# Kernel tuning notes

Measured on AMD Instinct MI355X. Metric: run time of the kernel, lower is better.

## Reference

```python
import jax, jax.numpy as jnp
import numpy as np

B, C, H, W = 8, 96, 224, 224
WS, SS, NH = 7, 3, 3          # window size, shift size, num heads
HD = C // NH                  # head dim = 32
N = WS * WS                   # tokens per window = 49
MLP_H = 4 * C
EPS = 1e-5


def _rel_pos_index():
    coords = np.stack(np.meshgrid(np.arange(WS), np.arange(WS), indexing='ij'))  # (2, ws, ws)
    cf = coords.reshape(2, -1)                       # (2, N)
    rel = cf[:, :, None] - cf[:, None, :]            # (2, N, N)
    rel = rel.transpose(1, 2, 0).copy()              # (N, N, 2)
    rel[:, :, 0] += WS - 1
    rel[:, :, 1] += WS - 1
    rel[:, :, 0] *= 2 * WS - 1
    return rel.sum(-1)                               # (N, N) int


def _attn_mask():
    # Swin shifted-window mask: (num_windows, N, N) with 0 / -100
    img = np.zeros((H, W), np.float32)
    cnt = 0
    for hs in (slice(0, -WS), slice(-WS, -SS), slice(-SS, None)):
        for ws_ in (slice(0, -WS), slice(-WS, -SS), slice(-SS, None)):
            img[hs, ws_] = cnt
            cnt += 1
    mw = img.reshape(H // WS, WS, W // WS, WS).transpose(0, 2, 1, 3).reshape(-1, N)
    m = mw[:, None, :] - mw[:, :, None]
    return np.where(m != 0, np.float32(-100.0), np.float32(0.0))


def setup_inputs() -> dict:
    key = jax.random.key(0)
    ks = jax.random.split(key, 8)
    s = 0.02
    return {
        "x": jax.random.normal(ks[0], (B, C, H, W), jnp.float32),
        "attn_mask": jnp.asarray(_attn_mask()),
        "norm1_g": jnp.ones((C,), jnp.float32),
        "norm1_b": jnp.zeros((C,), jnp.float32),
        "qkv_w": jax.random.normal(ks[1], (C, 3 * C), jnp.float32) * s,
        "qkv_b": jnp.zeros((3 * C,), jnp.float32),
        "rpb": jax.random.normal(ks[2], ((2 * WS - 1) ** 2, NH), jnp.float32) * s,
        "proj_w": jax.random.normal(ks[3], (C, C), jnp.float32) * s,
        "proj_b": jnp.zeros((C,), jnp.float32),
        "norm2_g": jnp.ones((C,), jnp.float32),
        "norm2_b": jnp.zeros((C,), jnp.float32),
        "fc1_w": jax.random.normal(ks[4], (C, MLP_H), jnp.float32) * s,
        "fc1_b": jnp.zeros((MLP_H,), jnp.float32),
        "fc2_w": jax.random.normal(ks[5], (MLP_H, C), jnp.float32) * s,
        "fc2_b": jnp.zeros((C,), jnp.float32),
    }


def _ln(x, g, b):
    mu = jnp.mean(x, axis=-1, keepdims=True)
    var = jnp.var(x, axis=-1, keepdims=True)
    return (x - mu) * jax.lax.rsqrt(var + EPS) * g + b


def reference(x, attn_mask, norm1_g, norm1_b, qkv_w, qkv_b, rpb, proj_w, proj_b,
              norm2_g, norm2_b, fc1_w, fc1_b, fc2_w, fc2_b):
    shortcut = x
    # (B,C,H,W) -> (B,HW,C) -> LN -> (B,H,W,C)
    xl = jnp.transpose(x, (0, 2, 3, 1)).reshape(B, H * W, C)
    xl = _ln(xl, norm1_g, norm1_b).reshape(B, H, W, C)
    # H,W divisible by WS: pad_r = pad_b = 0
    sx = jnp.roll(xl, (-SS, -SS), axis=(1, 2))
    # window partition -> (B*nW, N, C)
    xw = sx.reshape(B, H // WS, WS, W // WS, WS, C).transpose(0, 1, 3, 2, 4, 5).reshape(-1, N, C)
    B_ = xw.shape[0]
    nW = B_ // B
    qkv = (xw @ qkv_w + qkv_b).reshape(B_, N, 3, NH, HD).transpose(2, 0, 3, 1, 4)
    q = qkv[0] * (HD ** -0.5)
    k, v = qkv[1], qkv[2]
    attn = jnp.einsum('bhnd,bhmd->bhnm', q, k)           # (B_, NH, N, N)
    rel_idx = jnp.asarray(_rel_pos_index())
    bias = rpb[rel_idx.reshape(-1)].reshape(N, N, NH).transpose(2, 0, 1)  # (NH, N, N)
    attn = attn + bias[None]
    attn = attn.reshape(B, nW, NH, N, N) + attn_mask[None, :, None]
    attn = jax.nn.softmax(attn.reshape(B_, NH, N, N), axis=-1)
    out = jnp.einsum('bhnm,bhmd->bhnd', attn, v).transpose(0, 2, 1, 3).reshape(B_, N, C)
    out = out @ proj_w + proj_b
    # window reverse -> (B, H, W, C)
    out = out.reshape(B, H // WS, W // WS, WS, WS, C).transpose(0, 1, 3, 2, 4, 5).reshape(B, H, W, C)
    out = jnp.roll(out, (SS, SS), axis=(1, 2))
    # faithful to original: permute(0,1,3,2) then raw reshape to (B,C,H,W)
    out = jnp.transpose(out, (0, 1, 3, 2)).reshape(B, C, H, W)
    x1 = shortcut + out
    # MLP branch, faithful: permute(0,1,3,2) then raw reshape to (B,HW,C)
    xm = jnp.transpose(x1, (0, 1, 3, 2)).reshape(B, H * W, C)
    xm = _ln(xm, norm2_g, norm2_b)
    xm = jax.nn.gelu(xm @ fc1_w + fc1_b, approximate=False) @ fc2_w + fc2_b
    xm = xm.reshape(B, C, H, W)
    return x1 + xm
```

## Files before the change

### kernel.cpp

```cpp
#include <hip/hip_runtime.h>
#include <hip/hip_bf16.h>


typedef __attribute__((ext_vector_type(4))) float f32x4;
typedef __attribute__((ext_vector_type(8))) short s16x8;

constexpr int B_ = 8;
constexpr int M_ = 96 * 224 * 224;

__device__ __forceinline__ ushort f2bs(float f) {
    __hip_bfloat16 h = __float2bfloat16(f);
    ushort u; __builtin_memcpy(&u, &h, 2); return u;
}
__device__ __forceinline__ float bs2f(ushort u) {
    __hip_bfloat16 h; __builtin_memcpy(&h, &u, 2); return __bfloat162float(h);
}
__device__ __forceinline__ f32x4 mfma16(s16x8 a, s16x8 b, f32x4 c) {
    return __builtin_amdgcn_mfma_f32_16x16x32_bf16(a, b, c, 0, 0, 0);
}
__device__ __forceinline__ float gelu_f(float v) {
    float s  = v * 0.70710678118654752f;
    float as = fabsf(s);
    float t  = __builtin_amdgcn_rcpf(fmaf(0.3275911f, as, 1.0f));
    float p  = fmaf(fmaf(fmaf(fmaf(1.061405429f, t, -1.453152027f), t,
                   1.421413741f), t, -0.284496736f), t, 0.254829592f) * t;
    float y  = 1.0f - p * __expf(-s * s);
    float er = copysignf(y, s);
    return 0.5f * v * (1.0f + er);
}

__global__ __launch_bounds__(256) void prep_kernel(
    const float* __restrict__ qkvw, const float* __restrict__ projw,
    const float* __restrict__ w1,   const float* __restrict__ w2,
    ushort* __restrict__ wq, ushort* __restrict__ wp,
    ushort* __restrict__ wf1, ushort* __restrict__ wf2)
{
    int i = blockIdx.x * 256 + threadIdx.x;
    if (i < 27648) { int n = i / 96, k = i % 96;  wq[i]  = f2bs(qkvw[k * 288 + n]); }
    if (i < 9216)  { int n = i / 96, k = i % 96;  wp[i]  = f2bs(projw[k * 96 + n]); }
    if (i < 36864) {
        int n = i / 96,  k = i % 96;   wf1[i] = f2bs(w1[k * 384 + n]);
        int n2 = i / 384, k2 = i % 384; wf2[i] = f2bs(w2[k2 * 96 + n2]);
    }
}

__global__ __launch_bounds__(256) void attn_kernel(
    const float* __restrict__ x,
    const float* __restrict__ amask,
    const float* __restrict__ n1g, const float* __restrict__ n1b,
    const float* __restrict__ qkvb,
    const float* __restrict__ rpb,
    const float* __restrict__ projb,
    const ushort* __restrict__ wq, const ushort* __restrict__ wp,
    ushort* __restrict__ x1)
{
    __shared__ __align__(16) ushort T[64][104];
    __shared__ __align__(16) ushort K[64][104];
    __shared__ __align__(16) ushort vT[96][72];
    __shared__ __align__(16) ushort Pws[4][16][72];
    __shared__ float rpbs[512];

    const int tid  = threadIdx.x;
    const int wave = tid >> 6, lane = tid & 63;
    const int cu   = lane & 15;
    const int g4   = lane >> 4;
    const int gk8  = g4 << 3;
    const int gr4  = g4 << 2;

    const int blk = (blockIdx.x & 7) * 1024 + (blockIdx.x >> 3);
    const int b   = blk >> 10;
    const int wi  = blk & 1023;
    const int wh  = wi >> 5, ww = wi & 31;
    const int bM  = b * M_;
    const bool need_mask = (wh == 31) || (ww == 31);

    for (int i = tid; i < 507; i += 256) rpbs[i] = rpb[i];

    const int t49 = tid % 49;
    const int g5  = tid / 49;
    int hh_s = 0, wc_s = 0;
    if (tid < 245) {
        int i = t49 / 7, j = t49 % 7;
        hh_s = wh * 7 + i + 3; if (hh_s >= 224) hh_s -= 224;
        wc_s = ww * 7 + j + 3; if (wc_s >= 224) wc_s -= 224;
    }

    if (tid < 245) {
        const float* xp = x + bM + g5 * 50176 + hh_s * 224 + wc_s;
        ushort* dT = &T[t49][g5];
        #pragma unroll 4
        for (int c = g5; c < 96; c += 5) {
            *dT = f2bs(*xp);
            xp += 5 * 50176; dT += 5;
        }
    }
    {
        uint* z = (uint*)&T[49][0];
        for (int i = tid; i < 780; i += 256) z[i] = 0u;
    }
    __syncthreads();

    if (tid < 196) {
        int t = tid >> 2, s = tid & 3;
        float sum = 0.f, sq = 0.f;
        float vv[24];
        #pragma unroll
        for (int i = 0; i < 24; ++i) {
            vv[i] = bs2f(T[t][s * 24 + i]);
            sum += vv[i]; sq += vv[i] * vv[i];
        }
        sum += __shfl_xor(sum, 1); sq += __shfl_xor(sq, 1);
        sum += __shfl_xor(sum, 2); sq += __shfl_xor(sq, 2);
        float mu   = sum * (1.0f / 96.0f);
        float rstd = rsqrtf(sq * (1.0f / 96.0f) - mu * mu + 1e-5f);
        #pragma unroll
        for (int i = 0; i < 24; ++i) {
            int c = s * 24 + i;
            T[t][c] = f2bs((vv[i] - mu) * rstd * n1g[c] + n1b[c]);
        }
    }
    __syncthreads();

    const int ar = (wave << 4) | cu;
    const int tr = (wave << 4) + gr4;

    {
        s16x8 a0 = *(const s16x8*)&T[ar][gk8];
        s16x8 a1 = *(const s16x8*)&T[ar][32 + gk8];
        s16x8 a2 = *(const s16x8*)&T[ar][64 + gk8];
        f32x4 qreg[6];

        auto qkv_store = [&](int nt, f32x4 acc) {
            int nc = (nt << 4) | cu;
            float bias = qkvb[nc];
            if (nt < 6) {
                #pragma unroll
                for (int r = 0; r < 4; ++r)
                    qreg[nt][r] = (acc[r] + bias) * 0.17677669529663689f;
            } else if (nt < 12) {
                #pragma unroll
                for (int r = 0; r < 4; ++r) K[tr + r][nc - 96] = f2bs(acc[r] + bias);
            } else {
                int d = nc - 192;
                ushort4 pk;
                pk.x = f2bs(acc[0] + bias); pk.y = f2bs(acc[1] + bias);
                pk.z = f2bs(acc[2] + bias); pk.w = f2bs(acc[3] + bias);
                *(ushort4*)&vT[d][tr] = pk;
            }
        };

        s16x8 e0, e1, e2, o0, o1, o2;
        {
            const ushort* bp = wq + cu * 96 + gk8;
            e0 = *(const s16x8*)(bp);
            e1 = *(const s16x8*)(bp + 32);
            e2 = *(const s16x8*)(bp + 64);
        }
        #pragma unroll
        for (int p = 0; p < 9; ++p) {
            const int ntE = 2 * p, ntO = 2 * p + 1;
            {
                int nc = (ntO << 4) | cu;
                const ushort* bp = wq + nc * 96 + gk8;
                o0 = *(const s16x8*)(bp);
                o1 = *(const s16x8*)(bp + 32);
                o2 = *(const s16x8*)(bp + 64);
            }
            {
                f32x4 acc = {0.f, 0.f, 0.f, 0.f};
                acc = mfma16(a0, e0, acc);
                acc = mfma16(a1, e1, acc);
                acc = mfma16(a2, e2, acc);
                qkv_store(ntE, acc);
            }
            if (p < 8) {
                int nc = ((ntE + 2) << 4) | cu;
                const ushort* bp = wq + nc * 96 + gk8;
                e0 = *(const s16x8*)(bp);
                e1 = *(const s16x8*)(bp + 32);
                e2 = *(const s16x8*)(bp + 64);
            }
            {
                f32x4 acc = {0.f, 0.f, 0.f, 0.f};
                acc = mfma16(a0, o0, acc);
                acc = mfma16(a1, o1, acc);
                acc = mfma16(a2, o2, acc);
                qkv_store(ntO, acc);
            }
        }
        #pragma unroll
        for (int qn = 0; qn < 6; ++qn)
            #pragma unroll
            for (int r = 0; r < 4; ++r)
                T[tr + r][(qn << 4) | cu] = f2bs(qreg[qn][r]);
    }
    __syncthreads();

    int u7d[4], u7m[4];
    #pragma unroll
    for (int ut = 0; ut < 4; ++ut) {
        int u = (ut << 4) | cu;
        u7d[ut] = u / 7; u7m[ut] = u % 7;
    }
    s16x8 ones8;
    #pragma unroll
    for (int i = 0; i < 8; ++i) ones8[i] = (short)0x3F80;

    #pragma unroll
    for (int it = 0; it < 3; ++it) {
        const int hh = it;
        const int t0r = tr;

        s16x8 aq = *(const s16x8*)&T[ar][(hh << 5) + gk8];
        s16x8 bk0 = *(const s16x8*)&K[(0 << 4) | cu][(hh << 5) + gk8];
        s16x8 bk1 = *(const s16x8*)&K[(1 << 4) | cu][(hh << 5) + gk8];
        s16x8 bk2 = *(const s16x8*)&K[(2 << 4) | cu][(hh << 5) + gk8];
        s16x8 bk3 = *(const s16x8*)&K[(3 << 4) | cu][(hh << 5) + gk8];
        f32x4 z = {0.f, 0.f, 0.f, 0.f};
        f32x4 sa[4];
        sa[0] = mfma16(aq, bk0, z);
        sa[1] = mfma16(aq, bk1, z);
        sa[2] = mfma16(aq, bk2, z);
        sa[3] = mfma16(aq, bk3, z);

        #pragma unroll
        for (int ut = 0; ut < 4; ++ut) {
            int u = (ut << 4) | cu;
            #pragma unroll
            for (int r = 0; r < 4; ++r) {
                int t = t0r + r;
                float s = sa[ut][r];
                if (t < 49 && u < 49) {
                    int dr = t / 7 - u7d[ut] + 6, dc = t % 7 - u7m[ut] + 6;
                    s += rpbs[(dr * 13 + dc) * 3 + hh];
                    if (need_mask) s += amask[(wi * 49 + t) * 49 + u];
                } else if (u >= 49) {
                    s = -1e30f;
                }
                sa[ut][r] = s;
            }
        }
        #pragma unroll
        for (int r = 0; r < 4; ++r) {
            float m = fmaxf(fmaxf(sa[0][r], sa[1][r]), fmaxf(sa[2][r], sa[3][r]));
            m = fmaxf(m, __shfl_xor(m, 1)); m = fmaxf(m, __shfl_xor(m, 2));
            m = fmaxf(m, __shfl_xor(m, 4)); m = fmaxf(m, __shfl_xor(m, 8));
            sa[0][r] = __expf(sa[0][r] - m);
            sa[1][r] = __expf(sa[1][r] - m);
            sa[2][r] = __expf(sa[2][r] - m);
            sa[3][r] = __expf(sa[3][r] - m);
        }
        #pragma unroll
        for (int ut = 0; ut < 4; ++ut) {
            int u = (ut << 4) | cu;
            #pragma unroll
            for (int r = 0; r < 4; ++r) Pws[wave][gr4 + r][u] = f2bs(sa[ut][r]);
        }
        s16x8 pa0 = *(const s16x8*)&Pws[wave][cu][gk8];
        s16x8 pa1 = *(const s16x8*)&Pws[wave][cu][32 + gk8];
        f32x4 accd = {0.f, 0.f, 0.f, 0.f};
        accd = mfma16(pa0, ones8, accd);
        accd = mfma16(pa1, ones8, accd);
        int d0 = (hh << 5) + cu, d1 = d0 + 16;
        s16x8 bv00 = *(const s16x8*)&vT[d0][gk8];
        s16x8 bv01 = *(const s16x8*)&vT[d0][32 + gk8];
        s16x8 bv10 = *(const s16x8*)&vT[d1][gk8];
        s16x8 bv11 = *(const s16x8*)&vT[d1][32 + gk8];
        f32x4 acco0 = {0.f, 0.f, 0.f, 0.f}, acco1 = {0.f, 0.f, 0.f, 0.f};
        acco0 = mfma16(pa0, bv00, acco0);
        acco0 = mfma16(pa1, bv01, acco0);
        acco1 = mfma16(pa0, bv10, acco1);
        acco1 = mfma16(pa1, bv11, acco1);
        float inv[4];
        #pragma unroll
        for (int r = 0; r < 4; ++r) inv[r] = __builtin_amdgcn_rcpf(accd[r]);
        #pragma unroll
        for (int r = 0; r < 4; ++r) {
            T[t0r + r][(hh << 5) + cu]      = f2bs(acco0[r] * inv[r]);
            T[t0r + r][(hh << 5) + 16 + cu] = f2bs(acco1[r] * inv[r]);
        }
    }

    {
        s16x8 a0 = *(const s16x8*)&T[ar][gk8];
        s16x8 a1 = *(const s16x8*)&T[ar][32 + gk8];
        s16x8 a2 = *(const s16x8*)&T[ar][64 + gk8];

        s16x8 e0, e1, e2, o0, o1, o2;
        {
            const ushort* bp = wp + cu * 96 + gk8;
            e0 = *(const s16x8*)(bp);
            e1 = *(const s16x8*)(bp + 32);
            e2 = *(const s16x8*)(bp + 64);
        }
        #pragma unroll
        for (int p = 0; p < 3; ++p) {
            const int ntE = 2 * p, ntO = 2 * p + 1;
            {
                int nc = (ntO << 4) | cu;
                const ushort* bp = wp + nc * 96 + gk8;
                o0 = *(const s16x8*)(bp);
                o1 = *(const s16x8*)(bp + 32);
                o2 = *(const s16x8*)(bp + 64);
            }
            {
                int nc = (ntE << 4) | cu;
                f32x4 acc = {0.f, 0.f, 0.f, 0.f};
                acc = mfma16(a0, e0, acc);
                acc = mfma16(a1, e1, acc);
                acc = mfma16(a2, e2, acc);
                float bias = projb[nc];
                #pragma unroll
                for (int r = 0; r < 4; ++r) T[tr + r][nc] = f2bs(acc[r] + bias);
            }
            if (p < 2) {
                int nc = ((ntE + 2) << 4) | cu;
                const ushort* bp = wp + nc * 96 + gk8;
                e0 = *(const s16x8*)(bp);
                e1 = *(const s16x8*)(bp + 32);
                e2 = *(const s16x8*)(bp + 64);
            }
            {
                int nc = (ntO << 4) | cu;
                f32x4 acc = {0.f, 0.f, 0.f, 0.f};
                acc = mfma16(a0, o0, acc);
                acc = mfma16(a1, o1, acc);
                acc = mfma16(a2, o2, acc);
                float bias = projb[nc];
                #pragma unroll
                for (int r = 0; r < 4; ++r) T[tr + r][nc] = f2bs(acc[r] + bias);
            }
        }
    }
    __syncthreads();

    if (tid < 245) {
        const int base = bM + (hh_s * 96 + g5) * 224 + wc_s;
        const float* xp = x + base;
        ushort* dx = x1 + base;
        const ushort* Tp = &T[t49][g5];
        #pragma unroll 4
        for (int c = g5; c < 96; c += 5) {
            *dx = f2bs(*xp + bs2f(*Tp));
            xp += 5 * 224; dx += 5 * 224; Tp += 5;
        }
    }
}

__global__ __launch_bounds__(256) void transpose_kernel(
    const ushort* __restrict__ x1, ushort* __restrict__ x1p)
{
    __shared__ ushort tile[32][36];
    const int id      = blockIdx.x;
    const int tile_id = id % 49;
    const int slab    = id / 49;
    const int h0 = (tile_id / 7) * 32;
    const int w0 = (tile_id % 7) * 32;
    const ushort* src = x1  + slab * 50176;
    ushort*       dst = x1p + slab * 50176;

    const int i = threadIdx.x >> 3;
    const int j = (threadIdx.x & 7) * 4;

    *(ushort4*)&tile[i][j] = *(const ushort4*)&src[(h0 + i) * 224 + w0 + j];
    __syncthreads();
    ushort4 v;
    v.x = tile[j][i]; v.y = tile[j + 1][i]; v.z = tile[j + 2][i]; v.w = tile[j + 3][i];
    *(ushort4*)&dst[(w0 + i) * 224 + h0 + j] = v;
}

template <bool CLEAN>
__device__ __forceinline__ void ln_token(
    const ushort* __restrict__ xsrc, int tok, int gk8,
    const float* __restrict__ n2g, const float* __restrict__ n2b,
    s16x8& a0, s16x8& a1, s16x8& a2)
{
    float vals[24];
    if (CLEAN) {
        const ushort* base = xsrc + tok * 96 + gk8;
        s16x8 r0 = *(const s16x8*)(base);
        s16x8 r1 = *(const s16x8*)(base + 32);
        s16x8 r2 = *(const s16x8*)(base + 64);
        #pragma unroll
        for (int i = 0; i < 8; ++i) {
            vals[i]      = bs2f((ushort)r0[i]);
            vals[8 + i]  = bs2f((ushort)r1[i]);
            vals[16 + i] = bs2f((ushort)r2[i]);
        }
    } else {
        int bb = tok / 50176;
        int tl = tok % 50176;
        #pragma unroll
        for (int s = 0; s < 3; ++s)
            #pragma unroll
            for (int i = 0; i < 8; ++i) {
                int p = tl * 96 + gk8 + s * 32 + i;
                int c = p / 50176, rem = p % 50176;
                int w = rem / 224, h = rem % 224;
                vals[s * 8 + i] = bs2f(xsrc[bb * M_ + c * 50176 + h * 224 + w]);
            }
    }
    float sum = 0.f, sq = 0.f;
    #pragma unroll
    for (int i = 0; i < 24; ++i) { sum += vals[i]; sq += vals[i] * vals[i]; }
    sum += __shfl_xor(sum, 16); sq += __shfl_xor(sq, 16);
    sum += __shfl_xor(sum, 32); sq += __shfl_xor(sq, 32);
    float mu   = sum * (1.0f / 96.0f);
    float rstd = rsqrtf(sq * (1.0f / 96.0f) - mu * mu + 1e-5f);
    #pragma unroll
    for (int i = 0; i < 8; ++i) {
        int c0 = gk8 + i, c1 = gk8 + 32 + i, c2 = gk8 + 64 + i;
        a0[i] = (short)f2bs((vals[i]      - mu) * rstd * n2g[c0] + n2b[c0]);
        a1[i] = (short)f2bs((vals[8 + i]  - mu) * rstd * n2g[c1] + n2b[c1]);
        a2[i] = (short)f2bs((vals[16 + i] - mu) * rstd * n2g[c2] + n2b[c2]);
    }
}

template <bool CLEAN>
__global__ __launch_bounds__(256) void mlp_kernel(
    const ushort* __restrict__ xsrc,
    const ushort* __restrict__ x1flat,
    const float* __restrict__ n2g, const float* __restrict__ n2b,
    const float* __restrict__ b1v, const float* __restrict__ b2v,
    const ushort* __restrict__ wf1, const ushort* __restrict__ wf2,
    float* __restrict__ out)
{
    __shared__ __align__(16) ushort hS[4][2][32][40];

    const int tid  = threadIdx.x;
    const int wave = tid >> 6, lane = tid & 63;
    const int cu   = lane & 15;
    const int g4   = lane >> 4;
    const int gk8  = g4 << 3;
    const int gr4  = g4 << 2;
    const int t0g  = blockIdx.x * 128;
    const int tokA = t0g + (wave << 5) + cu;
    const int tokB = tokA + 16;

    s16x8 aA0, aA1, aA2, aB0, aB1, aB2;
    ln_token<CLEAN>(xsrc, tokA, gk8, n2g, n2b, aA0, aA1, aA2);
    ln_token<CLEAN>(xsrc, tokB, gk8, n2g, n2b, aB0, aB1, aB2);

    auto fc1_step = [&](int s, int buf) {
        #pragma unroll
        for (int half = 0; half < 2; ++half) {
            int nc = ((2 * s + half) << 4) | cu;
            const ushort* bp = wf1 + nc * 96 + gk8;
            s16x8 b0 = *(const s16x8*)(bp);
            s16x8 b1 = *(const s16x8*)(bp + 32);
            s16x8 b2 = *(const s16x8*)(bp + 64);
            float bias = b1v[nc];
            f32x4 accA = {0.f, 0.f, 0.f, 0.f};
            accA = mfma16(aA0, b0, accA);
            accA = mfma16(aA1, b1, accA);
            accA = mfma16(aA2, b2, accA);
            f32x4 accB = {0.f, 0.f, 0.f, 0.f};
            accB = mfma16(aB0, b0, accB);
            accB = mfma16(aB1, b1, accB);
            accB = mfma16(aB2, b2, accB);
            #pragma unroll
            for (int r = 0; r < 4; ++r) {
                hS[wave][buf][gr4 + r][(half << 4) | cu]      = f2bs(gelu_f(accA[r] + bias));
                hS[wave][buf][16 + gr4 + r][(half << 4) | cu] = f2bs(gelu_f(accB[r] + bias));
            }
        }
    };

    f32x4 oaccA[6], oaccB[6];
    #pragma unroll
    for (int nt2 = 0; nt2 < 6; ++nt2) {
        oaccA[nt2] = (f32x4){0.f, 0.f, 0.f, 0.f};
        oaccB[nt2] = (f32x4){0.f, 0.f, 0.f, 0.f};
    }

    fc1_step(0, 0);
    for (int s = 0; s < 12; ++s) {
        int buf = s & 1;
        s16x8 haA = *(const s16x8*)&hS[wave][buf][cu][gk8];
        s16x8 haB = *(const s16x8*)&hS[wave][buf][16 + cu][gk8];
        if (s < 11) fc1_step(s + 1, buf ^ 1);
        #pragma unroll
        for (int nt2 = 0; nt2 < 6; ++nt2) {
            int nc2 = (nt2 << 4) | cu;
            s16x8 bv = *(const s16x8*)&wf2[nc2 * 384 + s * 32 + gk8];
            oaccA[nt2] = mfma16(haA, bv, oaccA[nt2]);
            oaccB[nt2] = mfma16(haB, bv, oaccB[nt2]);
        }
    }

    const int trow = (wave << 5) + gr4;
    #pragma unroll
    for (int nt2 = 0; nt2 < 6; ++nt2) {
        int nc2 = (nt2 << 4) | cu;
        float bias = b2v[nc2];
        #pragma unroll
        for (int r = 0; r < 4; ++r) {
            int GA = (t0g + trow + r) * 96 + nc2;
            out[GA] = bias + oaccA[nt2][r] + bs2f(x1flat[GA]);
            int GB = GA + 16 * 96;
            out[GB] = bias + oaccB[nt2][r] + bs2f(x1flat[GB]);
        }
    }
}

extern "C" void kernel_launch(void* const* d_in, const int* in_sizes, int n_in,
                              void* d_out, int out_size, void* d_ws, size_t ws_size,
                              hipStream_t stream) {
    const float* x      = (const float*)d_in[0];
    const float* amask  = (const float*)d_in[1];
    const float* n1g    = (const float*)d_in[2];
    const float* n1b    = (const float*)d_in[3];
    const float* qkvw   = (const float*)d_in[4];
    const float* qkvb   = (const float*)d_in[5];
    const float* rpb    = (const float*)d_in[6];
    const float* projw  = (const float*)d_in[7];
    const float* projb  = (const float*)d_in[8];
    const float* n2g    = (const float*)d_in[9];
    const float* n2b    = (const float*)d_in[10];
    const float* w1     = (const float*)d_in[11];
    const float* b1     = (const float*)d_in[12];
    const float* w2     = (const float*)d_in[13];
    const float* b2     = (const float*)d_in[14];

    char* ws = (char*)d_ws;
    ushort* wq  = (ushort*)(ws);
    ushort* wp  = (ushort*)(ws + 55296);
    ushort* wf1 = (ushort*)(ws + 73728);
    ushort* wf2 = (ushort*)(ws + 147456);
    ushort* x1  = (ushort*)(ws + 262144);
    ushort* x1p = (ushort*)(ws + 77332480);
    float* out = (float*)d_out;

    const bool clean = (ws_size >= (size_t)154402816);

    prep_kernel<<<dim3(144), dim3(256), 0, stream>>>(qkvw, projw, w1, w2, wq, wp, wf1, wf2);

    attn_kernel<<<dim3(8192), dim3(256), 0, stream>>>(
        x, amask, n1g, n1b, qkvb, rpb, projb, wq, wp, x1);

    if (clean) {
        transpose_kernel<<<dim3(37632), dim3(256), 0, stream>>>(x1, x1p);
        mlp_kernel<true><<<dim3(3136), dim3(256), 0, stream>>>(
            x1p, x1, n2g, n2b, b1, b2, wf1, wf2, out);
    } else {
        mlp_kernel<false><<<dim3(3136), dim3(256), 0, stream>>>(
            x1, x1, n2g, n2b, b1, b2, wf1, wf2, out);
    }
}
```

Before: 612.5 us.

## Process two adjacent windows per attention block with register prefetch of next window

New measurement: 627.6 us. 2.5% more time.

```diff
diff --git a/kernel.cpp b/kernel.cpp
--- a/kernel.cpp
+++ b/kernel.cpp
@@ -44,7 +44,7 @@
     }
 }
 
-__global__ __launch_bounds__(256) void attn_kernel(
+__global__ __launch_bounds__(256, 3) void attn_kernel(
     const float* __restrict__ x,
     const float* __restrict__ amask,
     const float* __restrict__ n1g, const float* __restrict__ n1b,
@@ -67,134 +67,28 @@
     const int gk8  = g4 << 3;
     const int gr4  = g4 << 2;
 
-    const int blk = (blockIdx.x & 7) * 1024 + (blockIdx.x >> 3);
-    const int b   = blk >> 10;
-    const int wi  = blk & 1023;
-    const int wh  = wi >> 5, ww = wi & 31;
-    const int bM  = b * M_;
-    const bool need_mask = (wh == 31) || (ww == 31);
+    const int pblk = (blockIdx.x & 7) * 512 + (blockIdx.x >> 3);
+    const int b    = pblk >> 9;
+    const int pr   = pblk & 511;
+    const int wh   = pr >> 4;
+    const int ww0  = (pr & 15) << 1;
+    const int bM   = b * M_;
 
     for (int i = tid; i < 507; i += 256) rpbs[i] = rpb[i];
 
     const int t49 = tid % 49;
     const int g5  = tid / 49;
-    int hh_s = 0, wc_s = 0;
-    if (tid < 245) {
-        int i = t49 / 7, j = t49 % 7;
-        hh_s = wh * 7 + i + 3; if (hh_s >= 224) hh_s -= 224;
-        wc_s = ww * 7 + j + 3; if (wc_s >= 224) wc_s -= 224;
-    }
-
-    if (tid < 245) {
-        const float* xp = x + bM + g5 * 50176 + hh_s * 224 + wc_s;
-        ushort* dT = &T[t49][g5];
-        #pragma unroll 4
-        for (int c = g5; c < 96; c += 5) {
-            *dT = f2bs(*xp);
-            xp += 5 * 50176; dT += 5;
-        }
-    }
-    {
-        uint* z = (uint*)&T[49][0];
-        for (int i = tid; i < 780; i += 256) z[i] = 0u;
-    }
-    __syncthreads();
-
-    if (tid < 196) {
-        int t = tid >> 2, s = tid & 3;
-        float sum = 0.f, sq = 0.f;
-        float vv[24];
-        #pragma unroll
-        for (int i = 0; i < 24; ++i) {
-            vv[i] = bs2f(T[t][s * 24 + i]);
-            sum += vv[i]; sq += vv[i] * vv[i];
-        }
-        sum += __shfl_xor(sum, 1); sq += __shfl_xor(sq, 1);
-        sum += __shfl_xor(sum, 2); sq += __shfl_xor(sq, 2);
-        float mu   = sum * (1.0f / 96.0f);
-        float rstd = rsqrtf(sq * (1.0f / 96.0f) - mu * mu + 1e-5f);
-        #pragma unroll
-        for (int i = 0; i < 24; ++i) {
-            int c = s * 24 + i;
-            T[t][c] = f2bs((vv[i] - mu) * rstd * n1g[c] + n1b[c]);
-        }
-    }
-    __syncthreads();
+    const bool vld = tid < 245;
+    int hh_s = 0, wc0 = 0, wc1 = 0;
+    if (vld) {
+        int i7 = t49 / 7, j7 = t49 % 7;
+        hh_s = wh * 7 + i7 + 3;  if (hh_s >= 224) hh_s -= 224;
+        wc0  = ww0 * 7 + j7 + 3; if (wc0 >= 224) wc0 -= 224;
+        wc1  = wc0 + 7;          if (wc1 >= 224) wc1 -= 224;
+    }
 
     const int ar = (wave << 4) | cu;
     const int tr = (wave << 4) + gr4;
-
-    {
-        s16x8 a0 = *(const s16x8*)&T[ar][gk8];
-        s16x8 a1 = *(const s16x8*)&T[ar][32 + gk8];
-        s16x8 a2 = *(const s16x8*)&T[ar][64 + gk8];
-        f32x4 qreg[6];
-
-        auto qkv_store = [&](int nt, f32x4 acc) {
-            int nc = (nt << 4) | cu;
-            float bias = qkvb[nc];
-            if (nt < 6) {
-                #pragma unroll
-                for (int r = 0; r < 4; ++r)
-                    qreg[nt][r] = (acc[r] + bias) * 0.17677669529663689f;
-            } else if (nt < 12) {
-                #pragma unroll
-                for (int r = 0; r < 4; ++r) K[tr + r][nc - 96] = f2bs(acc[r] + bias);
-            } else {
-                int d = nc - 192;
-                ushort4 pk;
-                pk.x = f2bs(acc[0] + bias); pk.y = f2bs(acc[1] + bias);
-                pk.z = f2bs(acc[2] + bias); pk.w = f2bs(acc[3] + bias);
-                *(ushort4*)&vT[d][tr] = pk;
-            }
-        };
-
-        s16x8 e0, e1, e2, o0, o1, o2;
-        {
-            const ushort* bp = wq + cu * 96 + gk8;
-            e0 = *(const s16x8*)(bp);
-            e1 = *(const s16x8*)(bp + 32);
-            e2 = *(const s16x8*)(bp + 64);
-        }
-        #pragma unroll
-        for (int p = 0; p < 9; ++p) {
-            const int ntE = 2 * p, ntO = 2 * p + 1;
-            {
-                int nc = (ntO << 4) | cu;
-                const ushort* bp = wq + nc * 96 + gk8;
-                o0 = *(const s16x8*)(bp);
-                o1 = *(const s16x8*)(bp + 32);
-                o2 = *(const s16x8*)(bp + 64);
-            }
-            {
-                f32x4 acc = {0.f, 0.f, 0.f, 0.f};
-                acc = mfma16(a0, e0, acc);
-                acc = mfma16(a1, e1, acc);
-                acc = mfma16(a2, e2, acc);
-                qkv_store(ntE, acc);
-            }
-            if (p < 8) {
-                int nc = ((ntE + 2) << 4) | cu;
-                const ushort* bp = wq + nc * 96 + gk8;
-                e0 = *(const s16x8*)(bp);
-                e1 = *(const s16x8*)(bp + 32);
-                e2 = *(const s16x8*)(bp + 64);
-            }
-            {
-                f32x4 acc = {0.f, 0.f, 0.f, 0.f};
-                acc = mfma16(a0, o0, acc);
-                acc = mfma16(a1, o1, acc);
-                acc = mfma16(a2, o2, acc);
-                qkv_store(ntO, acc);
-            }
-        }
-        #pragma unroll
-        for (int qn = 0; qn < 6; ++qn)
-            #pragma unroll
-            for (int r = 0; r < 4; ++r)
-                T[tr + r][(qn << 4) | cu] = f2bs(qreg[qn][r]);
-    }
-    __syncthreads();
 
     int u7d[4], u7m[4];
     #pragma unroll
@@ -206,145 +100,289 @@
     #pragma unroll
     for (int i = 0; i < 8; ++i) ones8[i] = (short)0x3F80;
 
-    #pragma unroll
-    for (int it = 0; it < 3; ++it) {
-        const int hh = it;
-        const int t0r = tr;
-
-        s16x8 aq = *(const s16x8*)&T[ar][(hh << 5) + gk8];
-        s16x8 bk0 = *(const s16x8*)&K[(0 << 4) | cu][(hh << 5) + gk8];
-        s16x8 bk1 = *(const s16x8*)&K[(1 << 4) | cu][(hh << 5) + gk8];
-        s16x8 bk2 = *(const s16x8*)&K[(2 << 4) | cu][(hh << 5) + gk8];
-        s16x8 bk3 = *(const s16x8*)&K[(3 << 4) | cu][(hh << 5) + gk8];
-        f32x4 z = {0.f, 0.f, 0.f, 0.f};
-        f32x4 sa[4];
-        sa[0] = mfma16(aq, bk0, z);
-        sa[1] = mfma16(aq, bk1, z);
-        sa[2] = mfma16(aq, bk2, z);
-        sa[3] = mfma16(aq, bk3, z);
-
-        #pragma unroll
-        for (int ut = 0; ut < 4; ++ut) {
-            int u = (ut << 4) | cu;
-            #pragma unroll
-            for (int r = 0; r < 4; ++r) {
-                int t = t0r + r;
-                float s = sa[ut][r];
-                if (t < 49 && u < 49) {
-                    int dr = t / 7 - u7d[ut] + 6, dc = t % 7 - u7m[ut] + 6;
-                    s += rpbs[(dr * 13 + dc) * 3 + hh];
-                    if (need_mask) s += amask[(wi * 49 + t) * 49 + u];
-                } else if (u >= 49) {
-                    s = -1e30f;
-                }
-                sa[ut][r] = s;
-            }
-        }
-        #pragma unroll
-        for (int r = 0; r < 4; ++r) {
-            float m = fmaxf(fmaxf(sa[0][r], sa[1][r]), fmaxf(sa[2][r], sa[3][r]));
-            m = fmaxf(m, __shfl_xor(m, 1)); m = fmaxf(m, __shfl_xor(m, 2));
-            m = fmaxf(m, __shfl_xor(m, 4)); m = fmaxf(m, __shfl_xor(m, 8));
-            sa[0][r] = __expf(sa[0][r] - m);
-            sa[1][r] = __expf(sa[1][r] - m);
-            sa[2][r] = __expf(sa[2][r] - m);
-            sa[3][r] = __expf(sa[3][r] - m);
-        }
-        #pragma unroll
-        for (int ut = 0; ut < 4; ++ut) {
-            int u = (ut << 4) | cu;
-            #pragma unroll
-            for (int r = 0; r < 4; ++r) Pws[wave][gr4 + r][u] = f2bs(sa[ut][r]);
-        }
-        s16x8 pa0 = *(const s16x8*)&Pws[wave][cu][gk8];
-        s16x8 pa1 = *(const s16x8*)&Pws[wave][cu][32 + gk8];
-        f32x4 accd = {0.f, 0.f, 0.f, 0.f};
-        accd = mfma16(pa0, ones8, accd);
-        accd = mfma16(pa1, ones8, accd);
-        int d0 = (hh << 5) + cu, d1 = d0 + 16;
-        s16x8 bv00 = *(const s16x8*)&vT[d0][gk8];
-        s16x8 bv01 = *(const s16x8*)&vT[d0][32 + gk8];
-        s16x8 bv10 = *(const s16x8*)&vT[d1][gk8];
-        s16x8 bv11 = *(const s16x8*)&vT[d1][32 + gk8];
-        f32x4 acco0 = {0.f, 0.f, 0.f, 0.f}, acco1 = {0.f, 0.f, 0.f, 0.f};
-        acco0 = mfma16(pa0, bv00, acco0);
-        acco0 = mfma16(pa1, bv01, acco0);
-        acco1 = mfma16(pa0, bv10, acco1);
-        acco1 = mfma16(pa1, bv11, acco1);
-        float inv[4];
-        #pragma unroll
-        for (int r = 0; r < 4; ++r) inv[r] = __builtin_amdgcn_rcpf(accd[r]);
-        #pragma unroll
-        for (int r = 0; r < 4; ++r) {
-            T[t0r + r][(hh << 5) + cu]      = f2bs(acco0[r] * inv[r]);
-            T[t0r + r][(hh << 5) + 16 + cu] = f2bs(acco1[r] * inv[r]);
-        }
-    }
-
-    {
-        s16x8 a0 = *(const s16x8*)&T[ar][gk8];
-        s16x8 a1 = *(const s16x8*)&T[ar][32 + gk8];
-        s16x8 a2 = *(const s16x8*)&T[ar][64 + gk8];
-
-        s16x8 e0, e1, e2, o0, o1, o2;
+    float rT[20], rN[20];
+
+    if (vld) {
+        const float* xp = x + bM + g5 * 50176 + hh_s * 224 + wc0;
+        #pragma unroll
+        for (int k = 0; k < 20; ++k) {
+            if (g5 + 5 * k < 96) rT[k] = xp[0];
+            xp += 5 * 50176;
+        }
+    }
+
+    auto run_window = [&](const float (&tok)[20], float (&ntok)[20],
+                          int wc_s, int ww, bool pf, int wcn) {
+        const int wi = (wh << 5) | ww;
+        const bool need_mask = (wh == 31) || (ww == 31);
+
+        if (vld) {
+            ushort* dT = &T[t49][g5];
+            #pragma unroll
+            for (int k = 0; k < 20; ++k) {
+                if (g5 + 5 * k < 96) *dT = f2bs(tok[k]);
+                dT += 5;
+            }
+        }
         {
-            const ushort* bp = wp + cu * 96 + gk8;
-            e0 = *(const s16x8*)(bp);
-            e1 = *(const s16x8*)(bp + 32);
-            e2 = *(const s16x8*)(bp + 64);
-        }
-        #pragma unroll
-        for (int p = 0; p < 3; ++p) {
-            const int ntE = 2 * p, ntO = 2 * p + 1;
+            uint* z = (uint*)&T[49][0];
+            for (int i = tid; i < 780; i += 256) z[i] = 0u;
+        }
+        __syncthreads();
+
+        if (tid < 196) {
+            int t = tid >> 2, s = tid & 3;
+            float sum = 0.f, sq = 0.f;
+            float vv[24];
+            #pragma unroll
+            for (int i = 0; i < 24; ++i) {
+                vv[i] = bs2f(T[t][s * 24 + i]);
+                sum += vv[i]; sq += vv[i] * vv[i];
+            }
+            sum += __shfl_xor(sum, 1); sq += __shfl_xor(sq, 1);
+            sum += __shfl_xor(sum, 2); sq += __shfl_xor(sq, 2);
+            float mu   = sum * (1.0f / 96.0f);
+            float rstd = rsqrtf(sq * (1.0f / 96.0f) - mu * mu + 1e-5f);
+            #pragma unroll
+            for (int i = 0; i < 24; ++i) {
+                int c = s * 24 + i;
+                T[t][c] = f2bs((vv[i] - mu) * rstd * n1g[c] + n1b[c]);
+            }
+        }
+        __syncthreads();
+
+        {
+            s16x8 a0 = *(const s16x8*)&T[ar][gk8];
+            s16x8 a1 = *(const s16x8*)&T[ar][32 + gk8];
+            s16x8 a2 = *(const s16x8*)&T[ar][64 + gk8];
+            f32x4 qreg[6];
+
+            auto qkv_store = [&](int nt, f32x4 acc) {
+                int nc = (nt << 4) | cu;
+                float bias = qkvb[nc];
+                if (nt < 6) {
+                    #pragma unroll
+                    for (int r = 0; r < 4; ++r)
+                        qreg[nt][r] = (acc[r] + bias) * 0.17677669529663689f;
+                } else if (nt < 12) {
+                    #pragma unroll
+                    for (int r = 0; r < 4; ++r) K[tr + r][nc - 96] = f2bs(acc[r] + bias);
+                } else {
+                    int d = nc - 192;
+                    ushort4 pk;
+                    pk.x = f2bs(acc[0] + bias); pk.y = f2bs(acc[1] + bias);
+                    pk.z = f2bs(acc[2] + bias); pk.w = f2bs(acc[3] + bias);
+                    *(ushort4*)&vT[d][tr] = pk;
+                }
+            };
+
+            s16x8 e0, e1, e2, o0, o1, o2;
             {
-                int nc = (ntO << 4) | cu;
-                const ushort* bp = wp + nc * 96 + gk8;
-                o0 = *(const s16x8*)(bp);
-                o1 = *(const s16x8*)(bp + 32);
-                o2 = *(const s16x8*)(bp + 64);
-            }
-            {
-                int nc = (ntE << 4) | cu;
-                f32x4 acc = {0.f, 0.f, 0.f, 0.f};
-                acc = mfma16(a0, e0, acc);
-                acc = mfma16(a1, e1, acc);
-                acc = mfma16(a2, e2, acc);
-                float bias = projb[nc];
-                #pragma unroll
-                for (int r = 0; r < 4; ++r) T[tr + r][nc] = f2bs(acc[r] + bias);
-            }
-            if (p < 2) {
-                int nc = ((ntE + 2) << 4) | cu;
-                const ushort* bp = wp + nc * 96 + gk8;
+                const ushort* bp = wq + cu * 96 + gk8;
                 e0 = *(const s16x8*)(bp);
                 e1 = *(const s16x8*)(bp + 32);
                 e2 = *(const s16x8*)(bp + 64);
             }
+            #pragma unroll
+            for (int p = 0; p < 9; ++p) {
+                const int ntE = 2 * p, ntO = 2 * p + 1;
+                {
+                    int nc = (ntO << 4) | cu;
+                    const ushort* bp = wq + nc * 96 + gk8;
+                    o0 = *(const s16x8*)(bp);
+                    o1 = *(const s16x8*)(bp + 32);
+                    o2 = *(const s16x8*)(bp + 64);
+                }
+                {
+                    f32x4 acc = {0.f, 0.f, 0.f, 0.f};
+                    acc = mfma16(a0, e0, acc);
+                    acc = mfma16(a1, e1, acc);
+                    acc = mfma16(a2, e2, acc);
+                    qkv_store(ntE, acc);
+                }
+                if (p < 8) {
+                    int nc = ((ntE + 2) << 4) | cu;
+                    const ushort* bp = wq + nc * 96 + gk8;
+                    e0 = *(const s16x8*)(bp);
+                    e1 = *(const s16x8*)(bp + 32);
+                    e2 = *(const s16x8*)(bp + 64);
+                }
+                {
+                    f32x4 acc = {0.f, 0.f, 0.f, 0.f};
+                    acc = mfma16(a0, o0, acc);
+                    acc = mfma16(a1, o1, acc);
+                    acc = mfma16(a2, o2, acc);
+                    qkv_store(ntO, acc);
+                }
+            }
+            #pragma unroll
+            for (int qn = 0; qn < 6; ++qn)
+                #pragma unroll
+                for (int r = 0; r < 4; ++r)
+                    T[tr + r][(qn << 4) | cu] = f2bs(qreg[qn][r]);
+        }
+        __syncthreads();
+
+        if (pf && vld) {
+            const float* xp = x + bM + g5 * 50176 + hh_s * 224 + wcn;
+            #pragma unroll
+            for (int k = 0; k < 20; ++k) {
+                if (g5 + 5 * k < 96) ntok[k] = xp[0];
+                xp += 5 * 50176;
+            }
+        }
+        float rX[20];
+        if (vld) {
+            const float* xp = x + bM + (hh_s * 96 + g5) * 224 + wc_s;
+            #pragma unroll
+            for (int k = 0; k < 20; ++k) {
+                if (g5 + 5 * k < 96) rX[k] = xp[0];
+                xp += 5 * 224;
+            }
+        }
+
+        #pragma unroll
+        for (int it = 0; it < 3; ++it) {
+            const int hh = it;
+            const int t0r = tr;
+
+            s16x8 aq = *(const s16x8*)&T[ar][(hh << 5) + gk8];
+            s16x8 bk0 = *(const s16x8*)&K[(0 << 4) | cu][(hh << 5) + gk8];
+            s16x8 bk1 = *(const s16x8*)&K[(1 << 4) | cu][(hh << 5) + gk8];
+            s16x8 bk2 = *(const s16x8*)&K[(2 << 4) | cu][(hh << 5) + gk8];
+            s16x8 bk3 = *(const s16x8*)&K[(3 << 4) | cu][(hh << 5) + gk8];
+            f32x4 z = {0.f, 0.f, 0.f, 0.f};
+            f32x4 sa[4];
+            sa[0] = mfma16(aq, bk0, z);
+            sa[1] = mfma16(aq, bk1, z);
+            sa[2] = mfma16(aq, bk2, z);
+            sa[3] = mfma16(aq, bk3, z);
+
+            #pragma unroll
+            for (int ut = 0; ut < 4; ++ut) {
+                int u = (ut << 4) | cu;
+                #pragma unroll
+                for (int r = 0; r < 4; ++r) {
+                    int t = t0r + r;
+                    float s = sa[ut][r];
+                    if (t < 49 && u < 49) {
+                        int dr = t / 7 - u7d[ut] + 6, dc = t % 7 - u7m[ut] + 6;
+                        s += rpbs[(dr * 13 + dc) * 3 + hh];
+                        if (need_mask) s += amask[(wi * 49 + t) * 49 + u];
+                    } else if (u >= 49) {
+                        s = -1e30f;
+                    }
+                    sa[ut][r] = s;
+                }
+            }
+            #pragma unroll
+            for (int r = 0; r < 4; ++r) {
+                float m = fmaxf(fmaxf(sa[0][r], sa[1][r]), fmaxf(sa[2][r], sa[3][r]));
+                m = fmaxf(m, __shfl_xor(m, 1)); m = fmaxf(m, __shfl_xor(m, 2));
+                m = fmaxf(m, __shfl_xor(m, 4)); m = fmaxf(m, __shfl_xor(m, 8));
+                sa[0][r] = __expf(sa[0][r] - m);
+                sa[1][r] = __expf(sa[1][r] - m);
+                sa[2][r] = __expf(sa[2][r] - m);
+                sa[3][r] = __expf(sa[3][r] - m);
+            }
+            #pragma unroll
+            for (int ut = 0; ut < 4; ++ut) {
+                int u = (ut << 4) | cu;
+                #pragma unroll
+                for (int r = 0; r < 4; ++r) Pws[wave][gr4 + r][u] = f2bs(sa[ut][r]);
+            }
+            s16x8 pa0 = *(const s16x8*)&Pws[wave][cu][gk8];
+            s16x8 pa1 = *(const s16x8*)&Pws[wave][cu][32 + gk8];
+            f32x4 accd = {0.f, 0.f, 0.f, 0.f};
+            accd = mfma16(pa0, ones8, accd);
+            accd = mfma16(pa1, ones8, accd);
+            int d0 = (hh << 5) + cu, d1 = d0 + 16;
+            s16x8 bv00 = *(const s16x8*)&vT[d0][gk8];
+            s16x8 bv01 = *(const s16x8*)&vT[d0][32 + gk8];
+            s16x8 bv10 = *(const s16x8*)&vT[d1][gk8];
+            s16x8 bv11 = *(const s16x8*)&vT[d1][32 + gk8];
+            f32x4 acco0 = {0.f, 0.f, 0.f, 0.f}, acco1 = {0.f, 0.f, 0.f, 0.f};
+            acco0 = mfma16(pa0, bv00, acco0);
+            acco0 = mfma16(pa1, bv01, acco0);
+            acco1 = mfma16(pa0, bv10, acco1);
+            acco1 = mfma16(pa1, bv11, acco1);
+            float inv[4];
+            #pragma unroll
+            for (int r = 0; r < 4; ++r) inv[r] = __builtin_amdgcn_rcpf(accd[r]);
+            #pragma unroll
+            for (int r = 0; r < 4; ++r) {
+                T[t0r + r][(hh << 5) + cu]      = f2bs(acco0[r] * inv[r]);
+                T[t0r + r][(hh << 5) + 16 + cu] = f2bs(acco1[r] * inv[r]);
+            }
+        }
+
+        {
+            s16x8 a0 = *(const s16x8*)&T[ar][gk8];
+            s16x8 a1 = *(const s16x8*)&T[ar][32 + gk8];
+            s16x8 a2 = *(const s16x8*)&T[ar][64 + gk8];
+
+            s16x8 e0, e1, e2, o0, o1, o2;
             {
-                int nc = (ntO << 4) | cu;
-                f32x4 acc = {0.f, 0.f, 0.f, 0.f};
-                acc = mfma16(a0, o0, acc);
-                acc = mfma16(a1, o1, acc);
-                acc = mfma16(a2, o2, acc);
-                float bias = projb[nc];
-                #pragma unroll
-                for (int r = 0; r < 4; ++r) T[tr + r][nc] = f2bs(acc[r] + bias);
-            }
-        }
-    }
+                const ushort* bp = wp + cu * 96 + gk8;
+                e0 = *(const s16x8*)(bp);
+                e1 = *(const s16x8*)(bp + 32);
+                e2 = *(const s16x8*)(bp + 64);
+            }
+            #pragma unroll
+            for (int p = 0; p < 3; ++p) {
+                const int ntE = 2 * p, ntO = 2 * p + 1;
+                {
+                    int nc = (ntO << 4) | cu;
+                    const ushort* bp = wp + nc * 96 + gk8;
+                    o0 = *(const s16x8*)(bp);
+                    o1 = *(const s16x8*)(bp + 32);
+                    o2 = *(const s16x8*)(bp + 64);
+                }
+                {
+                    int nc = (ntE << 4) | cu;
+                    f32x4 acc = {0.f, 0.f, 0.f, 0.f};
+                    acc = mfma16(a0, e0, acc);
+                    acc = mfma16(a1, e1, acc);
+                    acc = mfma16(a2, e2, acc);
+                    float bias = projb[nc];
+                    #pragma unroll
+                    for (int r = 0; r < 4; ++r) T[tr + r][nc] = f2bs(acc[r] + bias);
+                }
+                if (p < 2) {
+                    int nc = ((ntE + 2) << 4) | cu;
+                    const ushort* bp = wp + nc * 96 + gk8;
+                    e0 = *(const s16x8*)(bp);
+                    e1 = *(const s16x8*)(bp + 32);
+                    e2 = *(const s16x8*)(bp + 64);
+                }
+                {
+                    int nc = (ntO << 4) | cu;
+                    f32x4 acc = {0.f, 0.f, 0.f, 0.f};
+                    acc = mfma16(a0, o0, acc);
+                    acc = mfma16(a1, o1, acc);
+                    acc = mfma16(a2, o2, acc);
+                    float bias = projb[nc];
+                    #pragma unroll
+                    for (int r = 0; r < 4; ++r) T[tr + r][nc] = f2bs(acc[r] + bias);
+                }
+            }
+        }
+        __syncthreads();
+
+        if (vld) {
+            ushort* dx = x1 + bM + (hh_s * 96 + g5) * 224 + wc_s;
+            const ushort* Tp = &T[t49][g5];
+            #pragma unroll
+            for (int k = 0; k < 20; ++k) {
+                if (g5 + 5 * k < 96) *dx = f2bs(rX[k] + bs2f(*Tp));
+                dx += 5 * 224; Tp += 5;
+            }
+        }
+    };
+
+    run_window(rT, rN, wc0, ww0, true, wc1);
     __syncthreads();
-
-    if (tid < 245) {
-        const int base = bM + (hh_s * 96 + g5) * 224 + wc_s;
-        const float* xp = x + base;
-        ushort* dx = x1 + base;
-        const ushort* Tp = &T[t49][g5];
-        #pragma unroll 4
-        for (int c = g5; c < 96; c += 5) {
-            *dx = f2bs(*xp + bs2f(*Tp));
-            xp += 5 * 224; dx += 5 * 224; Tp += 5;
-        }
-    }
+    run_window(rN, rT, wc1, ww0 + 1, false, 0);
 }
 
 __global__ __launch_bounds__(256) void transpose_kernel(
@@ -535,7 +573,7 @@
 
     prep_kernel<<<dim3(144), dim3(256), 0, stream>>>(qkvw, projw, w1, w2, wq, wp, wf1, wf2);
 
-    attn_kernel<<<dim3(8192), dim3(256), 0, stream>>>(
+    attn_kernel<<<dim3(4096), dim3(256), 0, stream>>>(
         x, amask, n1g, n1b, qkvb, rpb, projb, wq, wp, x1);
 
     if (clean) {
```
